# Optimization experiments

Measured on AMD Instinct MI355X. Metric: run time of the kernel, lower is better.

## Reference

```python
import jax, jax.numpy as jnp
import numpy as np

N = 10000        # num_nodes
D = 256          # num_attrs
AVG_DEG = 32
K = N // 2       # known nodes
ALPHA = 0.5
BETA = 0.5


def setup_inputs() -> dict:
    rng = np.random.default_rng(0)
    # random graph -> symmetric adjacency (duplicate edges coalesce by summation,
    # matching torch_geometric coalescing of edge weights)
    src = rng.integers(0, N, size=N * AVG_DEG)
    dst = rng.integers(0, N, size=N * AVG_DEG)
    A = np.zeros((N, N), dtype=np.float32)
    np.add.at(A, (src, dst), 1.0)
    np.add.at(A, (dst, src), 1.0)
    # symmetric normalized Laplacian: L = I - D^{-1/2} A D^{-1/2}
    deg = A.sum(axis=1)
    dinv = np.where(deg > 0, 1.0 / np.sqrt(np.maximum(deg, 1e-12)), 0.0).astype(np.float32)
    L = np.eye(N, dtype=np.float32) - (dinv[:, None] * A * dinv[None, :])

    raw_x = rng.standard_normal((N, D)).astype(np.float32)
    know = np.sort(rng.choice(N, size=K, replace=False)).astype(np.int64)
    mean = raw_x[know].mean(axis=0)                 # is_binary=False path
    out_k_init = (raw_x[know] - mean).astype(np.float32)  # std = 1
    x = np.zeros((N, D), dtype=np.float32)
    x[know] = raw_x[know]                           # nn.Parameter init

    theta = np.float32((1.0 - 1.0 / N) * (1.0 / ALPHA - 1.0))
    eta = np.float32((1.0 / BETA - 1.0) / ALPHA)
    return {
        "x": jnp.asarray(x),
        "L": jnp.asarray(L),
        "mean": jnp.asarray(mean),
        "out_k_init": jnp.asarray(out_k_init),
        "know_mask": jnp.asarray(know),
        "theta": jnp.asarray(theta),
        "eta": jnp.asarray(eta),
    }


def reference(x, L, mean, out_k_init, know_mask, theta, eta):
    n = x.shape[0]
    xn = x - mean  # std = 1
    # dirichlet loss: sum_f x_f^T L x_f == sum(xn * (L @ xn))
    dirichlet = jnp.sum(xn * (L @ xn))
    # avg_L = n/(n-1) I - 1/(n-1) 11^T  ->  quadratic form in closed form
    col = xn.sum(axis=0)  # [D]
    avg = (n / (n - 1)) * jnp.sum(xn * xn) - (1.0 / (n - 1)) * jnp.sum(col * col)
    # MSE with reduction='sum'
    recon = jnp.sum((xn[know_mask] - out_k_init) ** 2)
    return -(dirichlet + eta * recon + theta * avg)
```

## Files before the change

### kernel.cpp

```cpp
#include <hip/hip_runtime.h>


#define NN    10000
#define DD    256
#define PREPB 157
#define RECB  256
#define SBLK  1250
#define QCAP  2048

typedef float  f32x4 __attribute__((ext_vector_type(4)));
typedef short  s16x8 __attribute__((ext_vector_type(8)));
typedef short  s16x4 __attribute__((ext_vector_type(4)));

__device__ __forceinline__ unsigned short f2bf(float f) {
    union { float f; unsigned u; } c; c.f = f;
    unsigned u = c.u;
    u += 0x7fffu + ((u >> 16) & 1u);
    return (unsigned short)(u >> 16);
}
__device__ __forceinline__ float bfr(unsigned short h) {
    union { unsigned u; float f; } c; c.u = ((unsigned)h) << 16; return c.f;
}

__global__ __launch_bounds__(256) void prep_kernel(const float* __restrict__ x,
                                                   const float* __restrict__ mean,
                                                   const float* __restrict__ oki,
                                                   const int* __restrict__ know,
                                                   int K,
                                                   unsigned short* __restrict__ xnR,
                                                   float* __restrict__ csbuf,
                                                   float* __restrict__ ssbuf,
                                                   float* __restrict__ rbuf) {
    __shared__ __align__(16) unsigned short xs[64][264];
    __shared__ float red[8];
    const int t  = threadIdx.x;
    const int bb = blockIdx.x;
    if (bb < PREPB) {
        const int i0 = bb * 64;
        float ss = 0.f;
#pragma unroll
        for (int p = 0; p < 16; ++p) {
            const int li  = p * 256 + t;
            const int row = li >> 6;
            const int c4  = li & 63;
            const int gi  = i0 + row;
            f32x4 v = {0.f, 0.f, 0.f, 0.f};
            if (gi < NN) {
                const f32x4 xv = *(const f32x4*)(x + (size_t)gi * DD + c4 * 4);
                const f32x4 mv = *(const f32x4*)(mean + c4 * 4);
                v[0] = xv[0] - mv[0]; v[1] = xv[1] - mv[1];
                v[2] = xv[2] - mv[2]; v[3] = xv[3] - mv[3];
                ss += v[0]*v[0] + v[1]*v[1] + v[2]*v[2] + v[3]*v[3];
            }
            unsigned short h[4];
            h[0] = f2bf(v[0]); h[1] = f2bf(v[1]); h[2] = f2bf(v[2]); h[3] = f2bf(v[3]);
            *(s16x4*)&xs[row][c4 * 4] = *(const s16x4*)h;
        }
#pragma unroll
        for (int off = 32; off > 0; off >>= 1) ss += __shfl_xor(ss, off);
        if ((t & 63) == 0) red[t >> 6] = ss;
        __syncthreads();
        if (t == 0) ssbuf[bb] = red[0] + red[1] + red[2] + red[3];
        float css = 0.f;
        for (int ii = 0; ii < 64; ++ii) css += bfr(xs[ii][t]);
        csbuf[(size_t)bb * 256 + t] = css;
#pragma unroll
        for (int p = 0; p < 8; ++p) {
            const int row  = p * 8 + (t >> 5);
            const int colb = (t & 31) * 8;
            const int i = i0 + row;
            if (i < NN)
                *(s16x8*)(xnR + (size_t)i * DD + colb) = *(const s16x8*)&xs[row][colb];
        }
    } else {
        const int rb = bb - PREPB;
        const int w  = t >> 6, l = t & 63;
        const f32x4 mv = *(const f32x4*)(mean + l * 4);
        float s = 0.f;
        for (int r = rb * 4 + w; r < K; r += RECB * 4) {
            const int idx = know[r];
            const f32x4 xv = *(const f32x4*)(x   + (size_t)idx * DD + l * 4);
            const f32x4 ov = *(const f32x4*)(oki + (size_t)r   * DD + l * 4);
            const float d0 = xv[0] - mv[0] - ov[0];
            const float d1 = xv[1] - mv[1] - ov[1];
            const float d2 = xv[2] - mv[2] - ov[2];
            const float d3 = xv[3] - mv[3] - ov[3];
            s += d0*d0 + d1*d1 + d2*d2 + d3*d3;
        }
#pragma unroll
        for (int off = 32; off > 0; off >>= 1) s += __shfl_xor(s, off);
        if (l == 0) red[4 + w] = s;
        __syncthreads();
        if (t == 0) rbuf[rb] = red[4] + red[5] + red[6] + red[7];
    }
}

__global__ __launch_bounds__(256) void sdot_kernel(const float* __restrict__ L,
                                                   const unsigned short* __restrict__ xnR,
                                                   float* __restrict__ part) {
    __shared__ unsigned qidx[QCAP];
    __shared__ float    qval[QCAP];
    __shared__ __align__(16) unsigned short irw[8][264];
    __shared__ unsigned qcnt;
    __shared__ float red[4];
    const int t = threadIdx.x;
    const int b = blockIdx.x;
    const int ibt = 4 * b;
    const int ibb = NN - 8 - 4 * b;
    if (t == 0) qcnt = 0;
    {
        const int sr = t >> 5, sc = (t & 31) * 8;
        const int si = (sr < 4) ? (ibt + sr) : (ibb + sr);
        *(s16x8*)&irw[sr][sc] = *(const s16x8*)(xnR + (size_t)si * DD + sc);
    }
    __syncthreads();

#define ROWLEN(i_) ((NN - (((i_) >> 2) << 2) + 15) >> 4)
    const int l0 = ROWLEN(ibt);     const int l1 = ROWLEN(ibt + 1);
    const int l2 = ROWLEN(ibt + 2); const int l3 = ROWLEN(ibt + 3);
    const int l4 = ROWLEN(ibb + 4); const int l5 = ROWLEN(ibb + 5);
    const int l6 = ROWLEN(ibb + 6);
    const int pre1 = l0;        const int pre2 = pre1 + l1;
    const int pre3 = pre2 + l2; const int pre4 = pre3 + l3;
    const int pre5 = pre4 + l4; const int pre6 = pre5 + l5;
    const int pre7 = pre6 + l6;
    const int ntot = pre7 + ROWLEN(ibb + 7);
#undef ROWLEN

#define DECODE(g_)                                                             \
    int rr_ = 0, base_ = 0;                                                    \
    if ((g_) >= pre1) { rr_ = 1; base_ = pre1; }                               \
    if ((g_) >= pre2) { rr_ = 2; base_ = pre2; }                               \
    if ((g_) >= pre3) { rr_ = 3; base_ = pre3; }                               \
    if ((g_) >= pre4) { rr_ = 4; base_ = pre4; }                               \
    if ((g_) >= pre5) { rr_ = 5; base_ = pre5; }                               \
    if ((g_) >= pre6) { rr_ = 6; base_ = pre6; }                               \
    if ((g_) >= pre7) { rr_ = 7; base_ = pre7; }                               \
    const int i_ = (rr_ < 4) ? (ibt + rr_) : (ibb + rr_);                      \
    const int c_ = (((i_) >> 2) << 2) + (((g_) - base_) << 4);

#define ISSUE(V0_, V1_, V2_, V3_, g_) {                                        \
    if ((g_) < ntot) {                                                         \
        DECODE(g_)                                                             \
        const float* p_ = L + (size_t)i_ * NN + c_;                            \
        if (c_ + 16 <= NN) {                                                   \
            V0_ = *(const f32x4*)p_;        V1_ = *(const f32x4*)(p_ + 4);     \
            V2_ = *(const f32x4*)(p_ + 8);  V3_ = *(const f32x4*)(p_ + 12);    \
        } else {                                                               \
            _Pragma("unroll") for (int e_ = 0; e_ < 4; ++e_) {                 \
                V0_[e_] = (c_ + e_      < NN) ? p_[e_]      : 0.f;             \
                V1_[e_] = (c_ + e_ + 4  < NN) ? p_[e_ + 4]  : 0.f;             \
                V2_[e_] = (c_ + e_ + 8  < NN) ? p_[e_ + 8]  : 0.f;             \
                V3_[e_] = (c_ + e_ + 12 < NN) ? p_[e_ + 12] : 0.f;             \
            } } } }

#define PROC(V0_, V1_, V2_, V3_, g_) {                                         \
    if ((g_) < ntot) {                                                         \
        DECODE(g_)                                                             \
        _Pragma("unroll") for (int e_ = 0; e_ < 16; ++e_) {                    \
            const float v_ = (e_ < 4) ? V0_[e_] : (e_ < 8) ? V1_[e_ - 4]       \
                           : (e_ < 12) ? V2_[e_ - 8] : V3_[e_ - 12];           \
            const int j_ = c_ + e_;                                            \
            if (v_ != 0.f && j_ >= i_ && j_ < NN) {                            \
                const unsigned s_ = atomicAdd(&qcnt, 1u);                      \
                if (s_ < QCAP) {                                               \
                    qidx[s_] = ((unsigned)rr_ << 14) | (unsigned)j_;           \
                    qval[s_] = (j_ == i_) ? v_ : 2.f * v_;                     \
                } } } } }

    f32x4 A0, A1, A2, A3, B0, B1, B2, B3, C0, C1, C2, C3;
    int g = t;
    ISSUE(A0, A1, A2, A3, g)
    ISSUE(B0, B1, B2, B3, g + 256)
    ISSUE(C0, C1, C2, C3, g + 512)
    while (g < ntot) {
        PROC (A0, A1, A2, A3, g)
        ISSUE(A0, A1, A2, A3, g + 768)
        PROC (B0, B1, B2, B3, g + 256)
        ISSUE(B0, B1, B2, B3, g + 1024)
        PROC (C0, C1, C2, C3, g + 512)
        ISSUE(C0, C1, C2, C3, g + 1280)
        g += 768;
    }
#undef ISSUE
#undef PROC
#undef DECODE
    __syncthreads();
    const unsigned cnt = (qcnt < QCAP) ? qcnt : QCAP;

    const int grp = t >> 3;
    const int ln  = t & 7;
    const int cb  = ln * 32;
    float acc = 0.f;
    for (unsigned e = grp; e < cnt; e += 64) {
        const unsigned eB  = e + 32;
        const bool     hasB = (eB < cnt);
        const unsigned pkA = qidx[e];
        const unsigned pkB = hasB ? qidx[eB] : pkA;
        const int rrA = (int)(pkA >> 14), jA = (int)(pkA & 16383u);
        const int rrB = (int)(pkB >> 14), jB = (int)(pkB & 16383u);
        const unsigned short* pjA = xnR + (size_t)jA * DD + cb;
        const unsigned short* pjB = xnR + (size_t)jB * DD + cb;
        float dA = 0.f, dB = 0.f;
        {
            const s16x8 ja0 = *(const s16x8*)pjA,       ja1 = *(const s16x8*)(pjA + 8);
            const s16x8 jb0 = *(const s16x8*)pjB,       jb1 = *(const s16x8*)(pjB + 8);
            const s16x8 ia0 = *(const s16x8*)&irw[rrA][cb];
            const s16x8 ia1 = *(const s16x8*)&irw[rrA][cb + 8];
            const s16x8 ib0 = *(const s16x8*)&irw[rrB][cb];
            const s16x8 ib1 = *(const s16x8*)&irw[rrB][cb + 8];
#pragma unroll
            for (int k = 0; k < 8; ++k) {
                dA += bfr((unsigned short)ia0[k]) * bfr((unsigned short)ja0[k]);
                dB += bfr((unsigned short)ib0[k]) * bfr((unsigned short)jb0[k]);
            }
#pragma unroll
            for (int k = 0; k < 8; ++k) {
                dA += bfr((unsigned short)ia1[k]) * bfr((unsigned short)ja1[k]);
                dB += bfr((unsigned short)ib1[k]) * bfr((unsigned short)jb1[k]);
            }
        }
        {
            const s16x8 ja2 = *(const s16x8*)(pjA + 16), ja3 = *(const s16x8*)(pjA + 24);
            const s16x8 jb2 = *(const s16x8*)(pjB + 16), jb3 = *(const s16x8*)(pjB + 24);
            const s16x8 ia2 = *(const s16x8*)&irw[rrA][cb + 16];
            const s16x8 ia3 = *(const s16x8*)&irw[rrA][cb + 24];
            const s16x8 ib2 = *(const s16x8*)&irw[rrB][cb + 16];
            const s16x8 ib3 = *(const s16x8*)&irw[rrB][cb + 24];
#pragma unroll
            for (int k = 0; k < 8; ++k) {
                dA += bfr((unsigned short)ia2[k]) * bfr((unsigned short)ja2[k]);
                dB += bfr((unsigned short)ib2[k]) * bfr((unsigned short)jb2[k]);
            }
#pragma unroll
            for (int k = 0; k < 8; ++k) {
                dA += bfr((unsigned short)ia3[k]) * bfr((unsigned short)ja3[k]);
                dB += bfr((unsigned short)ib3[k]) * bfr((unsigned short)jb3[k]);
            }
        }
#pragma unroll
        for (int off = 1; off < 8; off <<= 1) {
            dA += __shfl_xor(dA, off);
            dB += __shfl_xor(dB, off);
        }
        if (ln == 0) {
            acc += qval[e] * dA;
            if (hasB) acc += qval[eB] * dB;
        }
    }
#pragma unroll
    for (int off = 32; off > 0; off >>= 1) acc += __shfl_xor(acc, off);
    if ((t & 63) == 0) red[t >> 6] = acc;
    __syncthreads();
    if (t == 0) part[b] = red[0] + red[1] + red[2] + red[3];
}

__global__ __launch_bounds__(256) void fin_kernel(const float* __restrict__ part,
                                                  const float* __restrict__ csbuf,
                                                  const float* __restrict__ ssbuf,
                                                  const float* __restrict__ rbuf,
                                                  const float* __restrict__ theta,
                                                  const float* __restrict__ eta,
                                                  float* __restrict__ out) {
    __shared__ float red[4][4];
    const int t = threadIdx.x;
    float sp = 0.f;
    for (int i = t; i < SBLK; i += 256) sp += part[i];
    float cs = 0.f;
    for (int bb = 0; bb < PREPB; ++bb) cs += csbuf[(size_t)bb * 256 + t];
    float c2 = cs * cs;
    float ssv = (t < PREPB) ? ssbuf[t] : 0.f;
    float rv  = rbuf[t];
#pragma unroll
    for (int off = 32; off > 0; off >>= 1) {
        sp  += __shfl_xor(sp, off);
        c2  += __shfl_xor(c2, off);
        ssv += __shfl_xor(ssv, off);
        rv  += __shfl_xor(rv, off);
    }
    if ((t & 63) == 0) {
        red[t >> 6][0] = sp; red[t >> 6][1] = c2;
        red[t >> 6][2] = ssv; red[t >> 6][3] = rv;
    }
    __syncthreads();
    if (t == 0) {
        float dir = 0.f, colsq = 0.f, ss = 0.f, rec = 0.f;
#pragma unroll
        for (int w = 0; w < 4; ++w) {
            dir += red[w][0]; colsq += red[w][1];
            ss  += red[w][2]; rec   += red[w][3];
        }
        const float n = (float)NN;
        const float avg = (n / (n - 1.f)) * ss - colsq / (n - 1.f);
        out[0] = -(dir + eta[0] * rec + theta[0] * avg);
    }
}

extern "C" void kernel_launch(void* const* d_in, const int* in_sizes, int n_in,
                              void* d_out, int out_size, void* d_ws, size_t ws_size,
                              hipStream_t stream) {
    const float* x     = (const float*)d_in[0];
    const float* L     = (const float*)d_in[1];
    const float* mean  = (const float*)d_in[2];
    const float* oki   = (const float*)d_in[3];
    const int*   know  = (const int*)d_in[4];
    const float* theta = (const float*)d_in[5];
    const float* eta   = (const float*)d_in[6];
    float* out = (float*)d_out;

    char* ws = (char*)d_ws;
    unsigned short* xnR = (unsigned short*)ws;
    float* part  = (float*)(ws + 6 * 1024 * 1024);
    float* csbuf = (float*)(ws + 7 * 1024 * 1024);
    float* ssbuf = (float*)(ws + 8 * 1024 * 1024);
    float* rbuf  = (float*)(ws + 8 * 1024 * 1024 + 4096);
    const int K = in_sizes[4];

    hipLaunchKernelGGL(prep_kernel, dim3(PREPB + RECB), dim3(256), 0, stream,
                       x, mean, oki, know, K, xnR, csbuf, ssbuf, rbuf);
    hipLaunchKernelGGL(sdot_kernel, dim3(SBLK), dim3(256), 0, stream, L, xnR, part);
    hipLaunchKernelGGL(fin_kernel,  dim3(1),    dim3(256), 0, stream,
                       part, csbuf, ssbuf, rbuf, theta, eta, out);
}
```

Baseline: 81.80 us.

## Split sparse scan and dot phases into separate kernels via global COO buffers

The fused scan-and-dot kernel is split in two. A scan kernel streams the upper triangle of L and writes the nonzero indices and values into per-block global COO lists. A separate dot kernel then reads those lists and computes the bf16 dot products. The scan also adds a quick OR test so that all-zero 16-element chunks skip the decode and per-element checks. The intent is to shrink the LDS footprint and register pressure of the scan kernel so more blocks stay resident while streaming L. The cost is an extra launch, a global write and read round trip of the COO data, and losing the ability to overlap the dot phase with the scan.

```diff
diff --git a/kernel.cpp b/kernel.cpp
--- a/kernel.cpp
+++ b/kernel.cpp
@@ -95,25 +95,19 @@
     }
 }
 
-__global__ __launch_bounds__(256) void sdot_kernel(const float* __restrict__ L,
-                                                   const unsigned short* __restrict__ xnR,
-                                                   float* __restrict__ part) {
-    __shared__ unsigned qidx[QCAP];
-    __shared__ float    qval[QCAP];
-    __shared__ __align__(16) unsigned short irw[8][264];
+__global__ __launch_bounds__(256) void scan_kernel(const float* __restrict__ L,
+                                                   unsigned* __restrict__ cooIdx,
+                                                   float* __restrict__ cooVal,
+                                                   unsigned* __restrict__ cnt) {
     __shared__ unsigned qcnt;
-    __shared__ float red[4];
     const int t = threadIdx.x;
     const int b = blockIdx.x;
     const int ibt = 4 * b;
     const int ibb = NN - 8 - 4 * b;
     if (t == 0) qcnt = 0;
-    {
-        const int sr = t >> 5, sc = (t & 31) * 8;
-        const int si = (sr < 4) ? (ibt + sr) : (ibb + sr);
-        *(s16x8*)&irw[sr][sc] = *(const s16x8*)(xnR + (size_t)si * DD + sc);
-    }
-    __syncthreads();
+    __syncthreads();
+    unsigned* gIdx = cooIdx + (size_t)b * QCAP;
+    float*    gVal = cooVal + (size_t)b * QCAP;
 
 #define ROWLEN(i_) ((NN - (((i_) >> 2) << 2) + 15) >> 4)
     const int l0 = ROWLEN(ibt);     const int l1 = ROWLEN(ibt + 1);
@@ -156,17 +150,22 @@
 
 #define PROC(V0_, V1_, V2_, V3_, g_) {                                         \
     if ((g_) < ntot) {                                                         \
-        DECODE(g_)                                                             \
-        _Pragma("unroll") for (int e_ = 0; e_ < 16; ++e_) {                    \
-            const float v_ = (e_ < 4) ? V0_[e_] : (e_ < 8) ? V1_[e_ - 4]       \
-                           : (e_ < 12) ? V2_[e_ - 8] : V3_[e_ - 12];           \
-            const int j_ = c_ + e_;                                            \
-            if (v_ != 0.f && j_ >= i_ && j_ < NN) {                            \
-                const unsigned s_ = atomicAdd(&qcnt, 1u);                      \
-                if (s_ < QCAP) {                                               \
-                    qidx[s_] = ((unsigned)rr_ << 14) | (unsigned)j_;           \
-                    qval[s_] = (j_ == i_) ? v_ : 2.f * v_;                     \
-                } } } } }
+        unsigned orv_ = 0u;                                                    \
+        _Pragma("unroll") for (int e_ = 0; e_ < 4; ++e_)                       \
+            orv_ |= __float_as_uint(V0_[e_]) | __float_as_uint(V1_[e_])        \
+                  | __float_as_uint(V2_[e_]) | __float_as_uint(V3_[e_]);       \
+        if (orv_ != 0u) {                                                      \
+            DECODE(g_)                                                         \
+            _Pragma("unroll") for (int e_ = 0; e_ < 16; ++e_) {                \
+                const float v_ = (e_ < 4) ? V0_[e_] : (e_ < 8) ? V1_[e_ - 4]   \
+                               : (e_ < 12) ? V2_[e_ - 8] : V3_[e_ - 12];       \
+                const int j_ = c_ + e_;                                        \
+                if (v_ != 0.f && j_ >= i_ && j_ < NN) {                        \
+                    const unsigned s_ = atomicAdd(&qcnt, 1u);                  \
+                    if (s_ < QCAP) {                                           \
+                        gIdx[s_] = ((unsigned)rr_ << 14) | (unsigned)j_;       \
+                        gVal[s_] = (j_ == i_) ? v_ : 2.f * v_;                 \
+                    } } } } } }
 
     f32x4 A0, A1, A2, A3, B0, B1, B2, B3, C0, C1, C2, C3;
     int g = t;
@@ -186,25 +185,47 @@
 #undef PROC
 #undef DECODE
     __syncthreads();
-    const unsigned cnt = (qcnt < QCAP) ? qcnt : QCAP;
+    if (t == 0) cnt[b] = (qcnt < QCAP) ? qcnt : QCAP;
+}
+
+__global__ __launch_bounds__(256) void dot_kernel(const unsigned* __restrict__ cooIdx,
+                                                  const float* __restrict__ cooVal,
+                                                  const unsigned* __restrict__ cnt,
+                                                  const unsigned short* __restrict__ xnR,
+                                                  float* __restrict__ part) {
+    __shared__ __align__(16) unsigned short irw[8][264];
+    __shared__ float red[4];
+    const int t = threadIdx.x;
+    const int b = blockIdx.x;
+    const int ibt = 4 * b;
+    const int ibb = NN - 8 - 4 * b;
+    {
+        const int sr = t >> 5, sc = (t & 31) * 8;
+        const int si = (sr < 4) ? (ibt + sr) : (ibb + sr);
+        *(s16x8*)&irw[sr][sc] = *(const s16x8*)(xnR + (size_t)si * DD + sc);
+    }
+    __syncthreads();
+    const unsigned n = cnt[b];
+    const unsigned* gIdx = cooIdx + (size_t)b * QCAP;
+    const float*    gVal = cooVal + (size_t)b * QCAP;
 
     const int grp = t >> 3;
     const int ln  = t & 7;
     const int cb  = ln * 32;
     float acc = 0.f;
-    for (unsigned e = grp; e < cnt; e += 64) {
-        const unsigned eB  = e + 32;
-        const bool     hasB = (eB < cnt);
-        const unsigned pkA = qidx[e];
-        const unsigned pkB = hasB ? qidx[eB] : pkA;
+    for (unsigned e = grp; e < n; e += 64) {
+        const unsigned eB   = e + 32;
+        const bool     hasB = (eB < n);
+        const unsigned pkA = gIdx[e];
+        const unsigned pkB = hasB ? gIdx[eB] : pkA;
         const int rrA = (int)(pkA >> 14), jA = (int)(pkA & 16383u);
         const int rrB = (int)(pkB >> 14), jB = (int)(pkB & 16383u);
         const unsigned short* pjA = xnR + (size_t)jA * DD + cb;
         const unsigned short* pjB = xnR + (size_t)jB * DD + cb;
         float dA = 0.f, dB = 0.f;
         {
-            const s16x8 ja0 = *(const s16x8*)pjA,       ja1 = *(const s16x8*)(pjA + 8);
-            const s16x8 jb0 = *(const s16x8*)pjB,       jb1 = *(const s16x8*)(pjB + 8);
+            const s16x8 ja0 = *(const s16x8*)pjA,        ja1 = *(const s16x8*)(pjA + 8);
+            const s16x8 jb0 = *(const s16x8*)pjB,        jb1 = *(const s16x8*)(pjB + 8);
             const s16x8 ia0 = *(const s16x8*)&irw[rrA][cb];
             const s16x8 ia1 = *(const s16x8*)&irw[rrA][cb + 8];
             const s16x8 ib0 = *(const s16x8*)&irw[rrB][cb];
@@ -244,8 +265,8 @@
             dB += __shfl_xor(dB, off);
         }
         if (ln == 0) {
-            acc += qval[e] * dA;
-            if (hasB) acc += qval[eB] * dB;
+            acc += gVal[e] * dA;
+            if (hasB) acc += gVal[eB] * dB;
         }
     }
 #pragma unroll
@@ -310,15 +331,21 @@
 
     char* ws = (char*)d_ws;
     unsigned short* xnR = (unsigned short*)ws;
-    float* part  = (float*)(ws + 6 * 1024 * 1024);
-    float* csbuf = (float*)(ws + 7 * 1024 * 1024);
-    float* ssbuf = (float*)(ws + 8 * 1024 * 1024);
-    float* rbuf  = (float*)(ws + 8 * 1024 * 1024 + 4096);
+    float*    part   = (float*)   (ws +  6u * 1024 * 1024);
+    float*    csbuf  = (float*)   (ws +  7u * 1024 * 1024);
+    float*    ssbuf  = (float*)   (ws +  8u * 1024 * 1024);
+    float*    rbuf   = (float*)   (ws +  8u * 1024 * 1024 + 4096);
+    unsigned* cooIdx = (unsigned*)(ws + 16u * 1024 * 1024);
+    float*    cooVal = (float*)   (ws + 28u * 1024 * 1024);
+    unsigned* cnt    = (unsigned*)(ws + 40u * 1024 * 1024);
     const int K = in_sizes[4];
 
     hipLaunchKernelGGL(prep_kernel, dim3(PREPB + RECB), dim3(256), 0, stream,
                        x, mean, oki, know, K, xnR, csbuf, ssbuf, rbuf);
-    hipLaunchKernelGGL(sdot_kernel, dim3(SBLK), dim3(256), 0, stream, L, xnR, part);
+    hipLaunchKernelGGL(scan_kernel, dim3(SBLK), dim3(256), 0, stream,
+                       L, cooIdx, cooVal, cnt);
+    hipLaunchKernelGGL(dot_kernel,  dim3(SBLK), dim3(256), 0, stream,
+                       cooIdx, cooVal, cnt, xnR, part);
     hipLaunchKernelGGL(fin_kernel,  dim3(1),    dim3(256), 0, stream,
                        part, csbuf, ssbuf, rbuf, theta, eta, out);
 }
```

After: 92.10 us. 1.13x slower.

## Interleave per-wave sparse dot products with dense Laplacian streaming

Applied to the files above, without the earlier changes.

Replaces the block-wide shared atomic queue with per-wavefront queues filled through ballot and popcount compaction, and skips fully-zero chunks with a wave ballot. Gathered bf16 dot products are now computed in small slices between the streaming loads of L, so the gather and FMA work overlaps the memory stream instead of running in a separate phase after a block barrier. The full-width L loads use nontemporal hints. Risks include per-wave queue overflow at 512 entries, extra ballot work per element, and weaker latency hiding if the interleaved dot work stalls the load pipeline.

```diff
diff --git a/kernel.cpp b/kernel.cpp
--- a/kernel.cpp
+++ b/kernel.cpp
@@ -6,7 +6,7 @@
 #define PREPB 157
 #define RECB  256
 #define SBLK  1250
-#define QCAP  2048
+#define WQC   512
 
 typedef float  f32x4 __attribute__((ext_vector_type(4)));
 typedef short  s16x8 __attribute__((ext_vector_type(8)));
@@ -20,6 +20,9 @@
 }
 __device__ __forceinline__ float bfr(unsigned short h) {
     union { unsigned u; float f; } c; c.u = ((unsigned)h) << 16; return c.f;
+}
+__device__ __forceinline__ f32x4 ldnt(const float* p) {
+    return __builtin_nontemporal_load((const f32x4*)p);
 }
 
 __global__ __launch_bounds__(256) void prep_kernel(const float* __restrict__ x,
@@ -98,22 +101,29 @@
 __global__ __launch_bounds__(256) void sdot_kernel(const float* __restrict__ L,
                                                    const unsigned short* __restrict__ xnR,
                                                    float* __restrict__ part) {
-    __shared__ unsigned qidx[QCAP];
-    __shared__ float    qval[QCAP];
+    __shared__ unsigned qidx[4][WQC];
+    __shared__ float    qval[4][WQC];
     __shared__ __align__(16) unsigned short irw[8][264];
-    __shared__ unsigned qcnt;
     __shared__ float red[4];
-    const int t = threadIdx.x;
-    const int b = blockIdx.x;
-    const int ibt = 4 * b;
-    const int ibb = NN - 8 - 4 * b;
-    if (t == 0) qcnt = 0;
+    const int t    = threadIdx.x;
+    const int b    = blockIdx.x;
+    const int wq   = t >> 6;
+    const int lane = t & 63;
+    const int ibt  = 4 * b;
+    const int ibb  = NN - 8 - 4 * b;
     {
         const int sr = t >> 5, sc = (t & 31) * 8;
         const int si = (sr < 4) ? (ibt + sr) : (ibb + sr);
         *(s16x8*)&irw[sr][sc] = *(const s16x8*)(xnR + (size_t)si * DD + sc);
     }
     __syncthreads();
+
+    const unsigned long long lmlt = (1ULL << lane) - 1ULL;
+    const int grp8 = lane >> 3;
+    const int ln8  = lane & 7;
+    const int cb   = ln8 * 32;
+    int wcnt = 0, wdone = 0;
+    float acc = 0.f;
 
 #define ROWLEN(i_) ((NN - (((i_) >> 2) << 2) + 15) >> 4)
     const int l0 = ROWLEN(ibt);     const int l1 = ROWLEN(ibt + 1);
@@ -144,8 +154,8 @@
         DECODE(g_)                                                             \
         const float* p_ = L + (size_t)i_ * NN + c_;                            \
         if (c_ + 16 <= NN) {                                                   \
-            V0_ = *(const f32x4*)p_;        V1_ = *(const f32x4*)(p_ + 4);     \
-            V2_ = *(const f32x4*)(p_ + 8);  V3_ = *(const f32x4*)(p_ + 12);    \
+            V0_ = ldnt(p_);      V1_ = ldnt(p_ + 4);                           \
+            V2_ = ldnt(p_ + 8);  V3_ = ldnt(p_ + 12);                          \
         } else {                                                               \
             _Pragma("unroll") for (int e_ = 0; e_ < 4; ++e_) {                 \
                 V0_[e_] = (c_ + e_      < NN) ? p_[e_]      : 0.f;             \
@@ -154,103 +164,94 @@
                 V3_[e_] = (c_ + e_ + 12 < NN) ? p_[e_ + 12] : 0.f;             \
             } } } }
 
-#define PROC(V0_, V1_, V2_, V3_, g_) {                                         \
+#define PROCW(V0_, V1_, V2_, V3_, g_) {                                        \
+    bool any_ = false;                                                         \
     if ((g_) < ntot) {                                                         \
+        unsigned orv_ = 0u;                                                    \
+        _Pragma("unroll") for (int e_ = 0; e_ < 4; ++e_)                       \
+            orv_ |= __float_as_uint(V0_[e_]) | __float_as_uint(V1_[e_])        \
+                  | __float_as_uint(V2_[e_]) | __float_as_uint(V3_[e_]);       \
+        any_ = (orv_ != 0u);                                                   \
+    }                                                                          \
+    if (__ballot(any_) != 0ULL) {                                              \
         DECODE(g_)                                                             \
         _Pragma("unroll") for (int e_ = 0; e_ < 16; ++e_) {                    \
             const float v_ = (e_ < 4) ? V0_[e_] : (e_ < 8) ? V1_[e_ - 4]       \
                            : (e_ < 12) ? V2_[e_ - 8] : V3_[e_ - 12];           \
             const int j_ = c_ + e_;                                            \
-            if (v_ != 0.f && j_ >= i_ && j_ < NN) {                            \
-                const unsigned s_ = atomicAdd(&qcnt, 1u);                      \
-                if (s_ < QCAP) {                                               \
-                    qidx[s_] = ((unsigned)rr_ << 14) | (unsigned)j_;           \
-                    qval[s_] = (j_ == i_) ? v_ : 2.f * v_;                     \
-                } } } } }
-
-    f32x4 A0, A1, A2, A3, B0, B1, B2, B3, C0, C1, C2, C3;
+            const bool p_ = ((g_) < ntot) && (v_ != 0.f) && (j_ >= i_)         \
+                            && (j_ < NN);                                      \
+            const unsigned long long m_ = __ballot(p_);                        \
+            if (p_) {                                                          \
+                const int slot_ = wcnt + (int)__popcll(m_ & lmlt);             \
+                if (slot_ < WQC) {                                             \
+                    qidx[wq][slot_] = ((unsigned)rr_ << 14) | (unsigned)j_;    \
+                    qval[wq][slot_] = (j_ == i_) ? v_ : 2.f * v_;              \
+                } }                                                            \
+            wcnt += (int)__popcll(m_);                                         \
+        }                                                                      \
+        if (wcnt > WQC) wcnt = WQC;                                            \
+    } }
+
+#define DOTSLICE(MAXN_) {                                                      \
+    int avail_ = wcnt - wdone;                                                 \
+    int take_  = avail_ < (MAXN_) ? avail_ : (MAXN_);                          \
+    if (take_ > 0) {                                                           \
+        float dsum_ = 0.f, vv_ = 0.f;                                          \
+        if (grp8 < take_) {                                                    \
+            const unsigned pk_ = qidx[wq][wdone + grp8];                       \
+            vv_ = qval[wq][wdone + grp8];                                      \
+            const int rr_ = (int)(pk_ >> 14), j_ = (int)(pk_ & 16383u);        \
+            const unsigned short* pj_ = xnR + (size_t)j_ * DD + cb;            \
+            const s16x8 j0_ = *(const s16x8*)pj_;                              \
+            const s16x8 j1_ = *(const s16x8*)(pj_ + 8);                        \
+            const s16x8 j2_ = *(const s16x8*)(pj_ + 16);                       \
+            const s16x8 j3_ = *(const s16x8*)(pj_ + 24);                       \
+            const s16x8 i0_ = *(const s16x8*)&irw[rr_][cb];                    \
+            const s16x8 i1_ = *(const s16x8*)&irw[rr_][cb + 8];                \
+            const s16x8 i2_ = *(const s16x8*)&irw[rr_][cb + 16];               \
+            const s16x8 i3_ = *(const s16x8*)&irw[rr_][cb + 24];               \
+            _Pragma("unroll") for (int k_ = 0; k_ < 8; ++k_) {                 \
+                dsum_ += bfr((unsigned short)i0_[k_]) * bfr((unsigned short)j0_[k_]); \
+                dsum_ += bfr((unsigned short)i1_[k_]) * bfr((unsigned short)j1_[k_]); \
+                dsum_ += bfr((unsigned short)i2_[k_]) * bfr((unsigned short)j2_[k_]); \
+                dsum_ += bfr((unsigned short)i3_[k_]) * bfr((unsigned short)j3_[k_]); \
+            } }                                                                \
+        dsum_ += __shfl_xor(dsum_, 1);                                         \
+        dsum_ += __shfl_xor(dsum_, 2);                                         \
+        dsum_ += __shfl_xor(dsum_, 4);                                         \
+        if (ln8 == 0 && grp8 < take_) acc += vv_ * dsum_;                      \
+        wdone += take_;                                                        \
+    } }
+
+    f32x4 A0 = {}, A1 = {}, A2 = {}, A3 = {};
+    f32x4 B0 = {}, B1 = {}, B2 = {}, B3 = {};
+    f32x4 C0 = {}, C1 = {}, C2 = {}, C3 = {};
     int g = t;
     ISSUE(A0, A1, A2, A3, g)
     ISSUE(B0, B1, B2, B3, g + 256)
     ISSUE(C0, C1, C2, C3, g + 512)
     while (g < ntot) {
-        PROC (A0, A1, A2, A3, g)
+        PROCW(A0, A1, A2, A3, g)
         ISSUE(A0, A1, A2, A3, g + 768)
-        PROC (B0, B1, B2, B3, g + 256)
+        DOTSLICE(8)
+        PROCW(B0, B1, B2, B3, g + 256)
         ISSUE(B0, B1, B2, B3, g + 1024)
-        PROC (C0, C1, C2, C3, g + 512)
+        DOTSLICE(8)
+        PROCW(C0, C1, C2, C3, g + 512)
         ISSUE(C0, C1, C2, C3, g + 1280)
+        DOTSLICE(8)
         g += 768;
     }
+    while (wdone < wcnt) DOTSLICE(8)
 #undef ISSUE
-#undef PROC
+#undef PROCW
+#undef DOTSLICE
 #undef DECODE
-    __syncthreads();
-    const unsigned cnt = (qcnt < QCAP) ? qcnt : QCAP;
-
-    const int grp = t >> 3;
-    const int ln  = t & 7;
-    const int cb  = ln * 32;
-    float acc = 0.f;
-    for (unsigned e = grp; e < cnt; e += 64) {
-        const unsigned eB  = e + 32;
-        const bool     hasB = (eB < cnt);
-        const unsigned pkA = qidx[e];
-        const unsigned pkB = hasB ? qidx[eB] : pkA;
-        const int rrA = (int)(pkA >> 14), jA = (int)(pkA & 16383u);
-        const int rrB = (int)(pkB >> 14), jB = (int)(pkB & 16383u);
-        const unsigned short* pjA = xnR + (size_t)jA * DD + cb;
-        const unsigned short* pjB = xnR + (size_t)jB * DD + cb;
-        float dA = 0.f, dB = 0.f;
-        {
-            const s16x8 ja0 = *(const s16x8*)pjA,       ja1 = *(const s16x8*)(pjA + 8);
-            const s16x8 jb0 = *(const s16x8*)pjB,       jb1 = *(const s16x8*)(pjB + 8);
-            const s16x8 ia0 = *(const s16x8*)&irw[rrA][cb];
-            const s16x8 ia1 = *(const s16x8*)&irw[rrA][cb + 8];
-            const s16x8 ib0 = *(const s16x8*)&irw[rrB][cb];
-            const s16x8 ib1 = *(const s16x8*)&irw[rrB][cb + 8];
-#pragma unroll
-            for (int k = 0; k < 8; ++k) {
-                dA += bfr((unsigned short)ia0[k]) * bfr((unsigned short)ja0[k]);
-                dB += bfr((unsigned short)ib0[k]) * bfr((unsigned short)jb0[k]);
-            }
-#pragma unroll
-            for (int k = 0; k < 8; ++k) {
-                dA += bfr((unsigned short)ia1[k]) * bfr((unsigned short)ja1[k]);
-                dB += bfr((unsigned short)ib1[k]) * bfr((unsigned short)jb1[k]);
-            }
-        }
-        {
-            const s16x8 ja2 = *(const s16x8*)(pjA + 16), ja3 = *(const s16x8*)(pjA + 24);
-            const s16x8 jb2 = *(const s16x8*)(pjB + 16), jb3 = *(const s16x8*)(pjB + 24);
-            const s16x8 ia2 = *(const s16x8*)&irw[rrA][cb + 16];
-            const s16x8 ia3 = *(const s16x8*)&irw[rrA][cb + 24];
-            const s16x8 ib2 = *(const s16x8*)&irw[rrB][cb + 16];
-            const s16x8 ib3 = *(const s16x8*)&irw[rrB][cb + 24];
-#pragma unroll
-            for (int k = 0; k < 8; ++k) {
-                dA += bfr((unsigned short)ia2[k]) * bfr((unsigned short)ja2[k]);
-                dB += bfr((unsigned short)ib2[k]) * bfr((unsigned short)jb2[k]);
-            }
-#pragma unroll
-            for (int k = 0; k < 8; ++k) {
-                dA += bfr((unsigned short)ia3[k]) * bfr((unsigned short)ja3[k]);
-                dB += bfr((unsigned short)ib3[k]) * bfr((unsigned short)jb3[k]);
-            }
-        }
-#pragma unroll
-        for (int off = 1; off < 8; off <<= 1) {
-            dA += __shfl_xor(dA, off);
-            dB += __shfl_xor(dB, off);
-        }
-        if (ln == 0) {
-            acc += qval[e] * dA;
-            if (hasB) acc += qval[eB] * dB;
-        }
-    }
+
 #pragma unroll
     for (int off = 32; off > 0; off >>= 1) acc += __shfl_xor(acc, off);
-    if ((t & 63) == 0) red[t >> 6] = acc;
+    if (lane == 0) red[wq] = acc;
     __syncthreads();
     if (t == 0) part[b] = red[0] + red[1] + red[2] + red[3];
 }
```

After: 111.6 us. 1.36x slower.
